# Optimization experiments

Measured on AMD Instinct MI355X. Metric: run time of the kernel, lower is better.

The kernel has to match this reference:

```python
import jax, jax.numpy as jnp
import numpy as np

L, H, C, V, B, T = 8, 12, 576, 16389, 2, 1024
HD = C // H


def _ln(h, w, b):
    mu = h.mean(-1, keepdims=True)
    var = ((h - mu) ** 2).mean(-1, keepdims=True)
    return (h - mu) * jax.lax.rsqrt(var + 1e-5) * w + b


def _forward(idx, wte, W_qkv, W_o, ln1_w, ln1_b, ln2_w, ln2_b, lambdas, W_gate, W_up, W_down, lnf_w, lnf_b):
    Bi, Ti = idx.shape
    scale = 1.0 / np.sqrt(HD).astype(np.float32)
    x = wte[idx]                          # [B,T,C] token embedding
    x0 = x                                # embed shortcut
    # value residual v1: third chunk of layer-0 c_attn applied to raw embeddings (no LN)
    qkv0 = x @ W_qkv[0].T                 # [B,T,3C]
    v1 = qkv0[..., 2 * C:].reshape(Bi, Ti, H, HD).transpose(0, 2, 1, 3)  # [B,H,T,hd]
    # ALiBi slopes: 1/x^(i+1), x = 256^(1/H)  ->  2^(-8(i+1)/H)
    slopes = 2.0 ** (-8.0 * jnp.arange(1, H + 1, dtype=jnp.float32) / H)
    r = jnp.arange(Ti)
    # (i - j).clamp(min=0) with i=cols, j=rows (zero on causal region, as in source)
    alibi = jnp.maximum(r[None, :] - r[:, None], 0).astype(jnp.float32)[None] * slopes[:, None, None]  # [H,T,T]
    causal = (r[None, :] <= r[:, None])[None, None]  # [1,1,T,T]

    def block(x, p):
        Wq, Wo, l1w, l1b, l2w, l2b, lam, Wg, Wu, Wd = p
        x = lam[0] * x + lam[1] * x0
        h = _ln(x, l1w, l1b)
        qkv = h @ Wq.T
        q, k, v = jnp.split(qkv, 3, axis=-1)
        q = q.reshape(Bi, Ti, H, HD).transpose(0, 2, 1, 3)
        k = k.reshape(Bi, Ti, H, HD).transpose(0, 2, 1, 3)
        v = v.reshape(Bi, Ti, H, HD).transpose(0, 2, 1, 3)
        v = 0.5 * v + 0.5 * v1               # value residual (fixed lambda)
        att = jnp.einsum('bhqd,bhkd->bhqk', q, k) * scale + alibi[None]
        att = jnp.where(causal, att, -jnp.inf)
        att = jax.nn.softmax(att, axis=-1)
        y = jnp.einsum('bhqk,bhkd->bhqd', att, v).transpose(0, 2, 1, 3).reshape(Bi, Ti, C)
        x = x + y @ Wo.T
        h2 = _ln(x, l2w, l2b)
        x = x + (jax.nn.gelu(h2 @ Wg.T, approximate=True) * (h2 @ Wu.T)) @ Wd.T  # GEGLU
        return x, None

    x, _ = jax.lax.scan(block, x, (W_qkv, W_o, ln1_w, ln1_b, ln2_w, ln2_b, lambdas, W_gate, W_up, W_down))
    x = _ln(x, lnf_w, lnf_b)
    logits = x @ wte.T                    # tied lm_head
    return 30.0 * jnp.tanh(logits / 30.0)  # logit_clamp


def setup_inputs() -> dict:
    key = jax.random.key(0)
    ks = jax.random.split(key, 8)
    s = 0.02
    return {
        'idx': jax.random.randint(ks[0], (B, T), 0, V, dtype=jnp.int32),
        'wte': s * jax.random.normal(ks[1], (V, C), jnp.float32),
        'W_qkv': s * jax.random.normal(ks[2], (L, 3 * C, C), jnp.float32),
        'W_o': s * jax.random.normal(ks[3], (L, C, C), jnp.float32),
        'ln1_w': jnp.ones((L, C), jnp.float32),
        'ln1_b': jnp.zeros((L, C), jnp.float32),
        'ln2_w': jnp.ones((L, C), jnp.float32),
        'ln2_b': jnp.zeros((L, C), jnp.float32),
        'lambdas': jnp.tile(jnp.array([1.0, 0.0], jnp.float32), (L, 1)),
        'W_gate': s * jax.random.normal(ks[4], (L, 2 * C, C), jnp.float32),
        'W_up': s * jax.random.normal(ks[5], (L, 2 * C, C), jnp.float32),
        'W_down': s * jax.random.normal(ks[6], (L, C, 2 * C), jnp.float32),
        'lnf_w': jnp.ones((C,), jnp.float32),
        'lnf_b': jnp.zeros((C,), jnp.float32),
    }


def reference(idx, wte, W_qkv, W_o, ln1_w, ln1_b, ln2_w, ln2_b, lambdas, W_gate, W_up, W_down, lnf_w, lnf_b):
    return _forward(idx, wte, W_qkv, W_o, ln1_w, ln1_b, ln2_w, ln2_b, lambdas, W_gate, W_up, W_down, lnf_w, lnf_b)
```

## Files before the change

kernel.cpp:

```cpp
#include <hip/hip_runtime.h>
#include <hip/hip_bf16.h>
#include <stdint.h>
#include <stddef.h>

#define NL 8
#define NH 12
#define CC 576
#define VV 16389
#define TT 1024
#define HD 48
#define BT 2048
#define C3 1728
#define C2 1152

typedef __attribute__((ext_vector_type(4))) float f32x4;
typedef __attribute__((ext_vector_type(8))) __bf16 bf16x8;
typedef __attribute__((ext_vector_type(8))) unsigned short u16x8;

static __device__ __forceinline__ unsigned short f2bf(float f) {
  __hip_bfloat16 h = __float2bfloat16(f);
  return __builtin_bit_cast(unsigned short, h);
}
static __device__ __forceinline__ float bf2f(unsigned short u) {
  __hip_bfloat16 h = __builtin_bit_cast(__hip_bfloat16, u);
  return __bfloat162float(h);
}
static __device__ __forceinline__ float gelu_tanh(float g) {
  float t = tanhf(0.7978845608028654f * (g + 0.044715f * g * g * g));
  return 0.5f * g * (1.f + t);
}

__global__ void cvt_kernel(const float* __restrict__ in, unsigned short* __restrict__ out, int n4) {
  int i = blockIdx.x * blockDim.x + threadIdx.x;
  int stride = gridDim.x * blockDim.x;
  for (; i < n4; i += stride) {
    float4 v = reinterpret_cast<const float4*>(in)[i];
    ushort4 o;
    o.x = f2bf(v.x); o.y = f2bf(v.y); o.z = f2bf(v.z); o.w = f2bf(v.w);
    reinterpret_cast<ushort4*>(out)[i] = o;
  }
}

__global__ void cvt_gu_kernel(const float* __restrict__ g, const float* __restrict__ u,
                              unsigned short* __restrict__ out, int n4) {
  int i = blockIdx.x * blockDim.x + threadIdx.x;
  int stride = gridDim.x * blockDim.x;
  const int per_l = C2 * (CC / 4);
  for (; i < n4; i += stride) {
    int l = i / per_l, rem = i - l * per_l;
    int j = rem / (CC / 4), c4 = rem - j * (CC / 4);
    float4 gv = reinterpret_cast<const float4*>(g)[i];
    float4 uv = reinterpret_cast<const float4*>(u)[i];
    ushort4 go, uo;
    go.x = f2bf(gv.x); go.y = f2bf(gv.y); go.z = f2bf(gv.z); go.w = f2bf(gv.w);
    uo.x = f2bf(uv.x); uo.y = f2bf(uv.y); uo.z = f2bf(uv.z); uo.w = f2bf(uv.w);
    size_t dst = ((size_t)l * 2 * C2 + 2 * j) * CC + c4 * 4;
    *reinterpret_cast<ushort4*>(out + dst) = go;
    *reinterpret_cast<ushort4*>(out + dst + CC) = uo;
  }
}

__global__ void embed_kernel(const int* __restrict__ idx, const float* __restrict__ wte,
                             float* __restrict__ x, float* __restrict__ x0,
                             unsigned short* __restrict__ xbf) {
  int t = blockIdx.x;
  int tok = idx[t];
  const float* src = wte + (size_t)tok * CC;
  size_t base = (size_t)t * CC;
  for (int c = threadIdx.x; c < CC; c += blockDim.x) {
    float v = src[c];
    x[base + c] = v;
    x0[base + c] = v;
    xbf[base + c] = f2bf(v);
  }
}

template<int MIX>
__global__ __launch_bounds__(256) void ln_kernel(
    const float* __restrict__ xin, const float* __restrict__ x0,
    const float* __restrict__ lam, const float* __restrict__ w,
    const float* __restrict__ b, float* __restrict__ xmix,
    unsigned short* __restrict__ hbf) {
  int row = blockIdx.x * 4 + (threadIdx.x >> 6);
  int lane = threadIdx.x & 63;
  size_t base = (size_t)row * CC;
  float lam0 = 1.f, lam1 = 0.f;
  if (MIX) { lam0 = lam[0]; lam1 = lam[1]; }
  float e[9];
  float s = 0.f;
#pragma unroll
  for (int j = 0; j < 9; ++j) {
    int c = lane + 64 * j;
    float v = xin[base + c];
    if (MIX) v = lam0 * v + lam1 * x0[base + c];
    e[j] = v; s += v;
  }
#pragma unroll
  for (int mm = 1; mm < 64; mm <<= 1) s += __shfl_xor(s, mm, 64);
  float mu = s * (1.f / 576.f);
  float var = 0.f;
#pragma unroll
  for (int j = 0; j < 9; ++j) { float d = e[j] - mu; var += d * d; }
#pragma unroll
  for (int mm = 1; mm < 64; mm <<= 1) var += __shfl_xor(var, mm, 64);
  float rstd = 1.f / sqrtf(var * (1.f / 576.f) + 1e-5f);
#pragma unroll
  for (int j = 0; j < 9; ++j) {
    int c = lane + 64 * j;
    if (MIX) xmix[base + c] = e[j];
    hbf[base + c] = f2bf((e[j] - mu) * rstd * w[c] + b[c]);
  }
}

template<int EPI, int BN>
__global__ __launch_bounds__(256) void gemm_bt(
    const unsigned short* __restrict__ X, const unsigned short* __restrict__ W,
    float* __restrict__ Cf, unsigned short* __restrict__ Cb,
    unsigned short* __restrict__ Cb2, const unsigned short* __restrict__ v1b,
    int N, int K) {
  constexpr int PB = BN / 32;
  constexpr int NI = BN / 32;
  __shared__ unsigned short As[128 * 64];
  __shared__ unsigned short Bs[BN * 64];
  const int tid = threadIdx.x;
  const int lane = tid & 63;
  const int wv = tid >> 6;
  const int wr = wv >> 1, wc = wv & 1;
  const int nwg = gridDim.x;
  const int bid = blockIdx.x;
  const int swz = (bid & 7) * (nwg >> 3) + (bid >> 3);
  const int m0 = (swz & 15) * 128;
  const int n0 = (swz >> 4) * BN;
  const int l15 = lane & 15, g = lane >> 4;
  const int trow = tid >> 3;
  const int tcb = (tid & 7) << 4;

  const unsigned short* xrow[4];
  const unsigned short* wrow[PB];
  int aoff[4], boff[PB];
#pragma unroll
  for (int p = 0; p < 4; ++p) {
    int r = p * 32 + trow;
    xrow[p] = X + (size_t)(m0 + r) * K + (tcb >> 1);
    aoff[p] = r * 128 + (tcb ^ ((trow & 7) << 4));
  }
#pragma unroll
  for (int p = 0; p < PB; ++p) {
    int r = p * 32 + trow;
    int rn = n0 + r; if (rn > N - 1) rn = N - 1;
    wrow[p] = W + (size_t)rn * K + (tcb >> 1);
    boff[p] = r * 128 + (tcb ^ ((trow & 7) << 4));
  }
  const int rdswz = (l15 & 7) << 4;

  f32x4 acc[4][NI];
  const f32x4 fz = {0.f, 0.f, 0.f, 0.f};
#pragma unroll
  for (int i = 0; i < 4; ++i)
#pragma unroll
    for (int j = 0; j < NI; ++j) acc[i][j] = fz;

  u16x8 stg[4 + PB];
#pragma unroll
  for (int p = 0; p < 4; ++p) stg[p] = *reinterpret_cast<const u16x8*>(xrow[p]);
#pragma unroll
  for (int p = 0; p < PB; ++p) stg[4 + p] = *reinterpret_cast<const u16x8*>(wrow[p]);

  for (int k0 = 0; k0 < K; k0 += 64) {
    __syncthreads();
#pragma unroll
    for (int p = 0; p < 4; ++p)
      *reinterpret_cast<u16x8*>(reinterpret_cast<char*>(As) + aoff[p]) = stg[p];
#pragma unroll
    for (int p = 0; p < PB; ++p)
      *reinterpret_cast<u16x8*>(reinterpret_cast<char*>(Bs) + boff[p]) = stg[4 + p];
    __syncthreads();
    if (k0 + 64 < K) {
#pragma unroll
      for (int p = 0; p < 4; ++p)
        stg[p] = *reinterpret_cast<const u16x8*>(xrow[p] + k0 + 64);
#pragma unroll
      for (int p = 0; p < PB; ++p)
        stg[4 + p] = *reinterpret_cast<const u16x8*>(wrow[p] + k0 + 64);
    }
#pragma unroll
    for (int kk = 0; kk < 2; ++kk) {
      const int kbyte = kk * 64 + g * 16;
      bf16x8 a[4], bb[NI];
#pragma unroll
      for (int mi = 0; mi < 4; ++mi) {
        int ar = wr * 64 + mi * 16 + l15;
        a[mi] = *reinterpret_cast<const bf16x8*>(
            reinterpret_cast<const char*>(As) + ar * 128 + (kbyte ^ rdswz));
      }
#pragma unroll
      for (int ni = 0; ni < NI; ++ni) {
        int br = wc * (BN / 2) + ni * 16 + l15;
        bb[ni] = *reinterpret_cast<const bf16x8*>(
            reinterpret_cast<const char*>(Bs) + br * 128 + (kbyte ^ rdswz));
      }
#pragma unroll
      for (int mi = 0; mi < 4; ++mi)
#pragma unroll
        for (int ni = 0; ni < NI; ++ni)
          acc[mi][ni] = __builtin_amdgcn_mfma_f32_16x16x32_bf16(a[mi], bb[ni], acc[mi][ni], 0, 0, 0);
    }
  }
#pragma unroll
  for (int mi = 0; mi < 4; ++mi) {
#pragma unroll
    for (int ni = 0; ni < NI; ++ni) {
      int gn = n0 + wc * (BN / 2) + ni * 16 + l15;
      int gm = m0 + wr * 64 + mi * 16 + g * 4;
#pragma unroll
      for (int r = 0; r < 4; ++r) {
        float v = acc[mi][ni][r];
        size_t row = (size_t)(gm + r);
        if (EPI == 5) {
          float partner = __shfl_xor(v, 1, 64);
          if ((l15 & 1) == 0 && gn < N)
            Cb[row * (N / 2) + (gn >> 1)] = f2bf(gelu_tanh(v) * partner);
        } else if (gn < N) {
          if (EPI == 0) Cf[row * N + gn] = v;
          else if (EPI == 1) Cf[row * N + gn] += v;
          else if (EPI == 2) Cf[row * N + gn] = 30.f * tanhf(v * (1.f / 30.f));
          else if (EPI == 3) Cb[row * N + gn] = f2bf(v);
          else if (EPI == 4) {
            if (gn < C2) Cb[row * C2 + gn] = f2bf(v);
            else Cb2[row * CC + (gn - C2)] = f2bf(0.5f * v + 0.5f * bf2f(v1b[row * CC + (gn - C2)]));
          }
        }
      }
    }
  }
}

__global__ __launch_bounds__(256) void attn_kernel(
    const unsigned short* __restrict__ qkb, const unsigned short* __restrict__ vmix,
    unsigned short* __restrict__ ybf) {
  __shared__ unsigned short Kl[64 * 56];
  __shared__ unsigned short Vt[48 * 72];
  __shared__ unsigned short Pl[4][16 * 72];
  const int bid = blockIdx.x;
  const int swz = (bid & 7) * 48 + (bid >> 3);
  const int qb = swz & 15, bh = swz >> 4;
  const int b = bh / NH, h = bh % NH;
  const int tid = threadIdx.x, lane = tid & 63, wv = tid >> 6;
  const int l15 = lane & 15, g = lane >> 4;
  const int rb = b * TT;
  const int q0 = qb * 64 + wv * 16;
  const float scale = 0.14433756729740643f;

  bf16x8 qa[2];
  {
    const unsigned short* qp = qkb + (size_t)(rb + q0 + l15) * C2 + h * HD;
    qa[0] = *reinterpret_cast<const bf16x8*>(qp + 8 * g);
    if (g < 2) qa[1] = *reinterpret_cast<const bf16x8*>(qp + 32 + 8 * g);
    else { u16x8 z = {0,0,0,0,0,0,0,0}; qa[1] = __builtin_bit_cast(bf16x8, z); }
  }

  float mrow[4], lrow[4];
  f32x4 o[3];
  const f32x4 fz = {0.f, 0.f, 0.f, 0.f};
#pragma unroll
  for (int r = 0; r < 4; ++r) { mrow[r] = -1e30f; lrow[r] = 0.f; }
  o[0] = fz; o[1] = fz; o[2] = fz;

  for (int kb = 0; kb <= qb; ++kb) {
    __syncthreads();
#pragma unroll
    for (int jj = 0; jj < 3; ++jj) {
      int fi = tid + 256 * jj;
      int r = fi / 12, dq = (fi % 12) * 4;
      *reinterpret_cast<ushort4*>(&Kl[r * 56 + dq]) =
          *reinterpret_cast<const ushort4*>(qkb + (size_t)(rb + kb * 64 + r) * C2 + CC + h * HD + dq);
    }
#pragma unroll
    for (int jj = 0; jj < 12; ++jj) {
      int e = tid + 256 * jj;
      int r = e / 48, d = e - r * 48;
      Vt[d * 72 + r] = vmix[(size_t)(rb + kb * 64 + r) * CC + h * HD + d];
    }
    __syncthreads();

    f32x4 s[4];
    s[0] = fz; s[1] = fz; s[2] = fz; s[3] = fz;
#pragma unroll
    for (int c = 0; c < 2; ++c) {
#pragma unroll
      for (int t4 = 0; t4 < 4; ++t4) {
        bf16x8 kf;
        if (c == 1 && g >= 2) {
          u16x8 z = {0,0,0,0,0,0,0,0};
          kf = __builtin_bit_cast(bf16x8, z);
        } else {
          kf = *reinterpret_cast<const bf16x8*>(&Kl[(t4 * 16 + l15) * 56 + c * 32 + 8 * g]);
        }
        s[t4] = __builtin_amdgcn_mfma_f32_16x16x32_bf16(qa[c], kf, s[t4], 0, 0, 0);
      }
    }
#pragma unroll
    for (int t4 = 0; t4 < 4; ++t4) s[t4] *= scale;
    if (kb == qb) {
#pragma unroll
      for (int t4 = 0; t4 < 4; ++t4) {
        int key = kb * 64 + t4 * 16 + l15;
#pragma unroll
        for (int r = 0; r < 4; ++r)
          if (key > q0 + g * 4 + r) s[t4][r] = -1e30f;
      }
    }
    float pv[4][4];
#pragma unroll
    for (int r = 0; r < 4; ++r) {
      float tm = fmaxf(fmaxf(s[0][r], s[1][r]), fmaxf(s[2][r], s[3][r]));
#pragma unroll
      for (int mm = 1; mm < 16; mm <<= 1) tm = fmaxf(tm, __shfl_xor(tm, mm, 64));
      float mnew = fmaxf(mrow[r], tm);
      float cf = __expf(mrow[r] - mnew);
      lrow[r] *= cf;
      o[0][r] *= cf; o[1][r] *= cf; o[2][r] *= cf;
      mrow[r] = mnew;
      float rs = 0.f;
#pragma unroll
      for (int t4 = 0; t4 < 4; ++t4) {
        float pe = __expf(s[t4][r] - mnew);
        pv[t4][r] = pe; rs += pe;
      }
#pragma unroll
      for (int mm = 1; mm < 16; mm <<= 1) rs += __shfl_xor(rs, mm, 64);
      lrow[r] += rs;
    }
#pragma unroll
    for (int t4 = 0; t4 < 4; ++t4)
#pragma unroll
      for (int r = 0; r < 4; ++r)
        Pl[wv][(g * 4 + r) * 72 + t4 * 16 + l15] = f2bf(pv[t4][r]);
#pragma unroll
    for (int c = 0; c < 2; ++c) {
      bf16x8 pa = *reinterpret_cast<const bf16x8*>(&Pl[wv][l15 * 72 + c * 32 + 8 * g]);
#pragma unroll
      for (int dt = 0; dt < 3; ++dt) {
        bf16x8 vb = *reinterpret_cast<const bf16x8*>(&Vt[(dt * 16 + l15) * 72 + c * 32 + 8 * g]);
        o[dt] = __builtin_amdgcn_mfma_f32_16x16x32_bf16(pa, vb, o[dt], 0, 0, 0);
      }
    }
  }
#pragma unroll
  for (int r = 0; r < 4; ++r) {
    float inv = 1.f / lrow[r];
    int tr = q0 + g * 4 + r;
#pragma unroll
    for (int dt = 0; dt < 3; ++dt)
      ybf[(size_t)(rb + tr) * CC + h * HD + dt * 16 + l15] = f2bf(o[dt][r] * inv);
  }
}

extern "C" void kernel_launch(void* const* d_in, const int* in_sizes, int n_in,
                              void* d_out, int out_size, void* d_ws, size_t ws_size,
                              hipStream_t stream) {
  (void)in_sizes; (void)n_in; (void)out_size; (void)ws_size;
  const int*   idx  = (const int*)d_in[0];
  const float* wte  = (const float*)d_in[1];
  const float* Wqkv = (const float*)d_in[2];
  const float* Wo   = (const float*)d_in[3];
  const float* ln1w = (const float*)d_in[4];
  const float* ln1b = (const float*)d_in[5];
  const float* ln2w = (const float*)d_in[6];
  const float* ln2b = (const float*)d_in[7];
  const float* lam  = (const float*)d_in[8];
  const float* Wg   = (const float*)d_in[9];
  const float* Wu   = (const float*)d_in[10];
  const float* Wd   = (const float*)d_in[11];
  const float* lnfw = (const float*)d_in[12];
  const float* lnfb = (const float*)d_in[13];
  float* out = (float*)d_out;

  char* ws = (char*)d_ws;
  size_t off = 0;
  auto alloc = [&](size_t bytes) -> void* {
    void* p = ws + off;
    off = (off + bytes + 255) & ~(size_t)255;
    return p;
  };
  unsigned short* wqkv_b = (unsigned short*)alloc((size_t)NL * C3 * CC * 2);
  unsigned short* wo_b   = (unsigned short*)alloc((size_t)NL * CC * CC * 2);
  unsigned short* wgu_b  = (unsigned short*)alloc((size_t)NL * 2 * C2 * CC * 2);
  unsigned short* wd_b   = (unsigned short*)alloc((size_t)NL * CC * C2 * 2);
  unsigned short* wte_b  = (unsigned short*)alloc((size_t)VV * CC * 2);
  float* x     = (float*)alloc((size_t)BT * CC * 4);
  float* x0    = (float*)alloc((size_t)BT * CC * 4);
  unsigned short* hb    = (unsigned short*)alloc((size_t)BT * CC * 2);
  unsigned short* qkb   = (unsigned short*)alloc((size_t)BT * C2 * 2);
  unsigned short* v1b   = (unsigned short*)alloc((size_t)BT * CC * 2);
  unsigned short* vmixb = (unsigned short*)alloc((size_t)BT * CC * 2);
  unsigned short* yb    = (unsigned short*)alloc((size_t)BT * CC * 2);
  unsigned short* gub   = (unsigned short*)alloc((size_t)BT * C2 * 2);

  auto cvt = [&](const float* in, unsigned short* o, size_t n) {
    cvt_kernel<<<dim3(2048), 256, 0, stream>>>(in, o, (int)(n / 4));
  };
  cvt(Wqkv, wqkv_b, (size_t)NL * C3 * CC);
  cvt(Wo,   wo_b,   (size_t)NL * CC * CC);
  cvt(Wd,   wd_b,   (size_t)NL * CC * C2);
  cvt(wte,  wte_b,  (size_t)VV * CC);
  cvt_gu_kernel<<<dim3(2048), 256, 0, stream>>>(Wg, Wu, wgu_b, NL * C2 * (CC / 4));

  embed_kernel<<<dim3(BT), 256, 0, stream>>>(idx, wte, x, x0, hb);

  auto nb = [](int N, int BN) { return (N + BN - 1) / BN; };
  gemm_bt<3, 64><<<dim3(16 * nb(CC, 64)), 256, 0, stream>>>(
      hb, wqkv_b + (size_t)C2 * CC, nullptr, v1b, nullptr, nullptr, CC, CC);

  for (int l = 0; l < NL; ++l) {
    ln_kernel<1><<<dim3(512), 256, 0, stream>>>(x, x0, lam + 2 * l, ln1w + l * CC, ln1b + l * CC, x, hb);
    gemm_bt<4, 128><<<dim3(16 * nb(C3, 128)), 256, 0, stream>>>(
        hb, wqkv_b + (size_t)l * C3 * CC, nullptr, qkb, vmixb, v1b, C3, CC);
    attn_kernel<<<dim3(16 * 24), 256, 0, stream>>>(qkb, vmixb, yb);
    gemm_bt<1, 64><<<dim3(16 * nb(CC, 64)), 256, 0, stream>>>(
        yb, wo_b + (size_t)l * CC * CC, x, nullptr, nullptr, nullptr, CC, CC);
    ln_kernel<0><<<dim3(512), 256, 0, stream>>>(x, nullptr, nullptr, ln2w + l * CC, ln2b + l * CC, nullptr, hb);
    gemm_bt<5, 128><<<dim3(16 * nb(2 * C2, 128)), 256, 0, stream>>>(
        hb, wgu_b + (size_t)l * 2 * C2 * CC, nullptr, gub, nullptr, nullptr, 2 * C2, CC);
    gemm_bt<1, 64><<<dim3(16 * nb(CC, 64)), 256, 0, stream>>>(
        gub, wd_b + (size_t)l * CC * C2, x, nullptr, nullptr, nullptr, CC, C2);
  }

  ln_kernel<0><<<dim3(512), 256, 0, stream>>>(x, nullptr, nullptr, lnfw, lnfb, nullptr, hb);
  gemm_bt<2, 128><<<dim3(16 * nb(VV, 128)), 256, 0, stream>>>(
      hb, wte_b, out, nullptr, nullptr, nullptr, VV, CC);
}
```

Measured before the change: 1.359 ms.

## Fuse LayerNorm into GEMM A-operand loads and use 64x64 tiles for narrow GEMMs

Removes the separate LayerNorm kernels. Each GEMM block now computes per-row mean and rstd for its M tile from the fp32 residual and applies normalisation while loading the A tile, converting to bf16 on the fly. The residual mix output goes to a ping-pong buffer to avoid read/write races across blocks. Narrow N=576 GEMMs switch to 64x64 tiles to double the grid size. The cost is redundant LN statistics and fp32 A loads in every N-tile block (up to 129 blocks for the lm_head), plus the extra reads of x0.

New measurement: 2.009 ms. +47.8%, slower.

```diff
diff --git a/kernel.cpp b/kernel.cpp
--- a/kernel.cpp
+++ b/kernel.cpp
@@ -75,53 +75,27 @@
   }
 }
 
-template<int MIX>
-__global__ __launch_bounds__(256) void ln_kernel(
-    const float* __restrict__ xin, const float* __restrict__ x0,
-    const float* __restrict__ lam, const float* __restrict__ w,
-    const float* __restrict__ b, float* __restrict__ xmix,
-    unsigned short* __restrict__ hbf) {
-  int row = blockIdx.x * 4 + (threadIdx.x >> 6);
-  int lane = threadIdx.x & 63;
-  size_t base = (size_t)row * CC;
-  float lam0 = 1.f, lam1 = 0.f;
-  if (MIX) { lam0 = lam[0]; lam1 = lam[1]; }
-  float e[9];
-  float s = 0.f;
-#pragma unroll
-  for (int j = 0; j < 9; ++j) {
-    int c = lane + 64 * j;
-    float v = xin[base + c];
-    if (MIX) v = lam0 * v + lam1 * x0[base + c];
-    e[j] = v; s += v;
-  }
-#pragma unroll
-  for (int mm = 1; mm < 64; mm <<= 1) s += __shfl_xor(s, mm, 64);
-  float mu = s * (1.f / 576.f);
-  float var = 0.f;
-#pragma unroll
-  for (int j = 0; j < 9; ++j) { float d = e[j] - mu; var += d * d; }
-#pragma unroll
-  for (int mm = 1; mm < 64; mm <<= 1) var += __shfl_xor(var, mm, 64);
-  float rstd = 1.f / sqrtf(var * (1.f / 576.f) + 1e-5f);
-#pragma unroll
-  for (int j = 0; j < 9; ++j) {
-    int c = lane + 64 * j;
-    if (MIX) xmix[base + c] = e[j];
-    hbf[base + c] = f2bf((e[j] - mu) * rstd * w[c] + b[c]);
-  }
-}
-
-template<int EPI, int BN>
+template<int EPI, int BM, int BN, int LNA>
 __global__ __launch_bounds__(256) void gemm_bt(
-    const unsigned short* __restrict__ X, const unsigned short* __restrict__ W,
+    const unsigned short* __restrict__ Xb, const float* __restrict__ Xf,
+    const float* __restrict__ X0, const float* __restrict__ lam,
+    const float* __restrict__ lnw, const float* __restrict__ lnb,
+    float* __restrict__ xmixout,
+    const unsigned short* __restrict__ W,
     float* __restrict__ Cf, unsigned short* __restrict__ Cb,
     unsigned short* __restrict__ Cb2, const unsigned short* __restrict__ v1b,
     int N, int K) {
+  constexpr int NMB = BT / BM;
+  constexpr int PA = BM / 32;
   constexpr int PB = BN / 32;
+  constexpr int MI = BM / 32;
   constexpr int NI = BN / 32;
-  __shared__ unsigned short As[128 * 64];
+  __shared__ unsigned short As[BM * 64];
   __shared__ unsigned short Bs[BN * 64];
+  __shared__ float MuS[(LNA > 0) ? BM : 1];
+  __shared__ float RsS[(LNA > 0) ? BM : 1];
+  __shared__ float WbS[(LNA > 0) ? CC : 1];
+  __shared__ float BbS[(LNA > 0) ? CC : 1];
   const int tid = threadIdx.x;
   const int lane = tid & 63;
   const int wv = tid >> 6;
@@ -129,19 +103,78 @@
   const int nwg = gridDim.x;
   const int bid = blockIdx.x;
   const int swz = (bid & 7) * (nwg >> 3) + (bid >> 3);
-  const int m0 = (swz & 15) * 128;
-  const int n0 = (swz >> 4) * BN;
+  const int m0 = (swz % NMB) * BM;
+  const int n0 = (swz / NMB) * BN;
   const int l15 = lane & 15, g = lane >> 4;
   const int trow = tid >> 3;
   const int tcb = (tid & 7) << 4;
 
-  const unsigned short* xrow[4];
+  float lam0 = 1.f, lam1 = 0.f;
+  if (LNA == 1) { lam0 = lam[0]; lam1 = lam[1]; }
+
+  if (LNA > 0) {
+    for (int c = tid; c < CC; c += 256) { WbS[c] = lnw[c]; BbS[c] = lnb[c]; }
+    for (int rr = 0; rr < BM / 4; ++rr) {
+      int r = wv * (BM / 4) + rr;
+      size_t grow = (size_t)(m0 + r) * CC;
+      float e[9];
+      float s = 0.f;
+#pragma unroll
+      for (int j = 0; j < 9; ++j) {
+        int c = lane + 64 * j;
+        float v = Xf[grow + c];
+        if (LNA == 1) v = lam0 * v + lam1 * X0[grow + c];
+        e[j] = v; s += v;
+      }
+#pragma unroll
+      for (int mm = 1; mm < 64; mm <<= 1) s += __shfl_xor(s, mm, 64);
+      float mu = s * (1.f / 576.f);
+      float var = 0.f;
+#pragma unroll
+      for (int j = 0; j < 9; ++j) { float d = e[j] - mu; var += d * d; }
+#pragma unroll
+      for (int mm = 1; mm < 64; mm <<= 1) var += __shfl_xor(var, mm, 64);
+      float rstd = 1.f / sqrtf(var * (1.f / 576.f) + 1e-5f);
+      if (lane == 0) { MuS[r] = mu; RsS[r] = rstd; }
+      if (LNA == 1 && n0 == 0) {
+#pragma unroll
+        for (int j = 0; j < 9; ++j) xmixout[grow + lane + 64 * j] = e[j];
+      }
+    }
+    __syncthreads();
+  }
+
+  auto ldA = [&](int p, int k) -> u16x8 {
+    int r = p * 32 + trow;
+    int c0 = (tid & 7) * 8;
+    if (LNA == 0) {
+      return *reinterpret_cast<const u16x8*>(Xb + (size_t)(m0 + r) * K + c0 + k);
+    } else {
+      size_t base = (size_t)(m0 + r) * CC + c0 + k;
+      float4 a0 = *reinterpret_cast<const float4*>(Xf + base);
+      float4 a1 = *reinterpret_cast<const float4*>(Xf + base + 4);
+      float ev[8] = {a0.x, a0.y, a0.z, a0.w, a1.x, a1.y, a1.z, a1.w};
+      if (LNA == 1) {
+        float4 b0 = *reinterpret_cast<const float4*>(X0 + base);
+        float4 b1 = *reinterpret_cast<const float4*>(X0 + base + 4);
+        float bv[8] = {b0.x, b0.y, b0.z, b0.w, b1.x, b1.y, b1.z, b1.w};
+#pragma unroll
+        for (int i = 0; i < 8; ++i) ev[i] = lam0 * ev[i] + lam1 * bv[i];
+      }
+      float mu = MuS[r], rs = RsS[r];
+      union { u16x8 v; unsigned short u[8]; } o;
+#pragma unroll
+      for (int i = 0; i < 8; ++i)
+        o.u[i] = f2bf((ev[i] - mu) * rs * WbS[c0 + k + i] + BbS[c0 + k + i]);
+      return o.v;
+    }
+  };
+
   const unsigned short* wrow[PB];
-  int aoff[4], boff[PB];
-#pragma unroll
-  for (int p = 0; p < 4; ++p) {
+  int aoff[PA], boff[PB];
+#pragma unroll
+  for (int p = 0; p < PA; ++p) {
     int r = p * 32 + trow;
-    xrow[p] = X + (size_t)(m0 + r) * K + (tcb >> 1);
     aoff[p] = r * 128 + (tcb ^ ((trow & 7) << 4));
   }
 #pragma unroll
@@ -153,43 +186,42 @@
   }
   const int rdswz = (l15 & 7) << 4;
 
-  f32x4 acc[4][NI];
+  f32x4 acc[MI][NI];
   const f32x4 fz = {0.f, 0.f, 0.f, 0.f};
 #pragma unroll
-  for (int i = 0; i < 4; ++i)
+  for (int i = 0; i < MI; ++i)
 #pragma unroll
     for (int j = 0; j < NI; ++j) acc[i][j] = fz;
 
-  u16x8 stg[4 + PB];
-#pragma unroll
-  for (int p = 0; p < 4; ++p) stg[p] = *reinterpret_cast<const u16x8*>(xrow[p]);
-#pragma unroll
-  for (int p = 0; p < PB; ++p) stg[4 + p] = *reinterpret_cast<const u16x8*>(wrow[p]);
+  u16x8 stg[PA + PB];
+#pragma unroll
+  for (int p = 0; p < PA; ++p) stg[p] = ldA(p, 0);
+#pragma unroll
+  for (int p = 0; p < PB; ++p) stg[PA + p] = *reinterpret_cast<const u16x8*>(wrow[p]);
 
   for (int k0 = 0; k0 < K; k0 += 64) {
     __syncthreads();
 #pragma unroll
-    for (int p = 0; p < 4; ++p)
+    for (int p = 0; p < PA; ++p)
       *reinterpret_cast<u16x8*>(reinterpret_cast<char*>(As) + aoff[p]) = stg[p];
 #pragma unroll
     for (int p = 0; p < PB; ++p)
-      *reinterpret_cast<u16x8*>(reinterpret_cast<char*>(Bs) + boff[p]) = stg[4 + p];
+      *reinterpret_cast<u16x8*>(reinterpret_cast<char*>(Bs) + boff[p]) = stg[PA + p];
     __syncthreads();
     if (k0 + 64 < K) {
 #pragma unroll
-      for (int p = 0; p < 4; ++p)
-        stg[p] = *reinterpret_cast<const u16x8*>(xrow[p] + k0 + 64);
+      for (int p = 0; p < PA; ++p) stg[p] = ldA(p, k0 + 64);
 #pragma unroll
       for (int p = 0; p < PB; ++p)
-        stg[4 + p] = *reinterpret_cast<const u16x8*>(wrow[p] + k0 + 64);
+        stg[PA + p] = *reinterpret_cast<const u16x8*>(wrow[p] + k0 + 64);
     }
 #pragma unroll
     for (int kk = 0; kk < 2; ++kk) {
       const int kbyte = kk * 64 + g * 16;
-      bf16x8 a[4], bb[NI];
-#pragma unroll
-      for (int mi = 0; mi < 4; ++mi) {
-        int ar = wr * 64 + mi * 16 + l15;
+      bf16x8 a[MI], bb[NI];
+#pragma unroll
+      for (int mi = 0; mi < MI; ++mi) {
+        int ar = wr * (BM / 2) + mi * 16 + l15;
         a[mi] = *reinterpret_cast<const bf16x8*>(
             reinterpret_cast<const char*>(As) + ar * 128 + (kbyte ^ rdswz));
       }
@@ -200,18 +232,18 @@
             reinterpret_cast<const char*>(Bs) + br * 128 + (kbyte ^ rdswz));
       }
 #pragma unroll
-      for (int mi = 0; mi < 4; ++mi)
+      for (int mi = 0; mi < MI; ++mi)
 #pragma unroll
         for (int ni = 0; ni < NI; ++ni)
           acc[mi][ni] = __builtin_amdgcn_mfma_f32_16x16x32_bf16(a[mi], bb[ni], acc[mi][ni], 0, 0, 0);
     }
   }
 #pragma unroll
-  for (int mi = 0; mi < 4; ++mi) {
+  for (int mi = 0; mi < MI; ++mi) {
 #pragma unroll
     for (int ni = 0; ni < NI; ++ni) {
       int gn = n0 + wc * (BN / 2) + ni * 16 + l15;
-      int gm = m0 + wr * 64 + mi * 16 + g * 4;
+      int gm = m0 + wr * (BM / 2) + mi * 16 + g * 4;
 #pragma unroll
       for (int r = 0; r < 4; ++r) {
         float v = acc[mi][ni][r];
@@ -388,8 +420,10 @@
   unsigned short* wgu_b  = (unsigned short*)alloc((size_t)NL * 2 * C2 * CC * 2);
   unsigned short* wd_b   = (unsigned short*)alloc((size_t)NL * CC * C2 * 2);
   unsigned short* wte_b  = (unsigned short*)alloc((size_t)VV * CC * 2);
-  float* x     = (float*)alloc((size_t)BT * CC * 4);
-  float* x0    = (float*)alloc((size_t)BT * CC * 4);
+  float* xe  = (float*)alloc((size_t)BT * CC * 4);
+  float* x0  = (float*)alloc((size_t)BT * CC * 4);
+  float* xb1 = (float*)alloc((size_t)BT * CC * 4);
+  float* xb2 = (float*)alloc((size_t)BT * CC * 4);
   unsigned short* hb    = (unsigned short*)alloc((size_t)BT * CC * 2);
   unsigned short* qkb   = (unsigned short*)alloc((size_t)BT * C2 * 2);
   unsigned short* v1b   = (unsigned short*)alloc((size_t)BT * CC * 2);
@@ -406,27 +440,34 @@
   cvt(wte,  wte_b,  (size_t)VV * CC);
   cvt_gu_kernel<<<dim3(2048), 256, 0, stream>>>(Wg, Wu, wgu_b, NL * C2 * (CC / 4));
 
-  embed_kernel<<<dim3(BT), 256, 0, stream>>>(idx, wte, x, x0, hb);
+  embed_kernel<<<dim3(BT), 256, 0, stream>>>(idx, wte, xe, x0, hb);
 
   auto nb = [](int N, int BN) { return (N + BN - 1) / BN; };
-  gemm_bt<3, 64><<<dim3(16 * nb(CC, 64)), 256, 0, stream>>>(
-      hb, wqkv_b + (size_t)C2 * CC, nullptr, v1b, nullptr, nullptr, CC, CC);
-
+  gemm_bt<3, 64, 64, 0><<<dim3(32 * nb(CC, 64)), 256, 0, stream>>>(
+      hb, nullptr, nullptr, nullptr, nullptr, nullptr, nullptr,
+      wqkv_b + (size_t)C2 * CC, nullptr, v1b, nullptr, nullptr, CC, CC);
+
+  float* cur = xe;
+  float* nxt = xb1;
   for (int l = 0; l < NL; ++l) {
-    ln_kernel<1><<<dim3(512), 256, 0, stream>>>(x, x0, lam + 2 * l, ln1w + l * CC, ln1b + l * CC, x, hb);
-    gemm_bt<4, 128><<<dim3(16 * nb(C3, 128)), 256, 0, stream>>>(
-        hb, wqkv_b + (size_t)l * C3 * CC, nullptr, qkb, vmixb, v1b, C3, CC);
+    gemm_bt<4, 128, 128, 1><<<dim3(16 * nb(C3, 128)), 256, 0, stream>>>(
+        nullptr, cur, x0, lam + 2 * l, ln1w + l * CC, ln1b + l * CC, nxt,
+        wqkv_b + (size_t)l * C3 * CC, nullptr, qkb, vmixb, v1b, C3, CC);
     attn_kernel<<<dim3(16 * 24), 256, 0, stream>>>(qkb, vmixb, yb);
-    gemm_bt<1, 64><<<dim3(16 * nb(CC, 64)), 256, 0, stream>>>(
-        yb, wo_b + (size_t)l * CC * CC, x, nullptr, nullptr, nullptr, CC, CC);
-    ln_kernel<0><<<dim3(512), 256, 0, stream>>>(x, nullptr, nullptr, ln2w + l * CC, ln2b + l * CC, nullptr, hb);
-    gemm_bt<5, 128><<<dim3(16 * nb(2 * C2, 128)), 256, 0, stream>>>(
-        hb, wgu_b + (size_t)l * 2 * C2 * CC, nullptr, gub, nullptr, nullptr, 2 * C2, CC);
-    gemm_bt<1, 64><<<dim3(16 * nb(CC, 64)), 256, 0, stream>>>(
-        gub, wd_b + (size_t)l * CC * C2, x, nullptr, nullptr, nullptr, CC, C2);
-  }
-
-  ln_kernel<0><<<dim3(512), 256, 0, stream>>>(x, nullptr, nullptr, lnfw, lnfb, nullptr, hb);
-  gemm_bt<2, 128><<<dim3(16 * nb(VV, 128)), 256, 0, stream>>>(
-      hb, wte_b, out, nullptr, nullptr, nullptr, VV, CC);
-}
+    gemm_bt<1, 64, 64, 0><<<dim3(32 * nb(CC, 64)), 256, 0, stream>>>(
+        yb, nullptr, nullptr, nullptr, nullptr, nullptr, nullptr,
+        wo_b + (size_t)l * CC * CC, nxt, nullptr, nullptr, nullptr, CC, CC);
+    gemm_bt<5, 128, 128, 2><<<dim3(16 * nb(2 * C2, 128)), 256, 0, stream>>>(
+        nullptr, nxt, nullptr, nullptr, ln2w + l * CC, ln2b + l * CC, nullptr,
+        wgu_b + (size_t)l * 2 * C2 * CC, nullptr, gub, nullptr, nullptr, 2 * C2, CC);
+    gemm_bt<1, 64, 64, 0><<<dim3(32 * nb(CC, 64)), 256, 0, stream>>>(
+        gub, nullptr, nullptr, nullptr, nullptr, nullptr, nullptr,
+        wd_b + (size_t)l * CC * C2, nxt, nullptr, nullptr, nullptr, CC, C2);
+    cur = nxt;
+    nxt = (cur == xb1) ? xb2 : xb1;
+  }
+
+  gemm_bt<2, 128, 128, 2><<<dim3(16 * nb(VV, 128)), 256, 0, stream>>>(
+      nullptr, cur, nullptr, nullptr, lnfw, lnfb, nullptr,
+      wte_b, out, nullptr, nullptr, nullptr, VV, CC);
+}
```

## Double-buffer attention K/V tiles, schedule heavy query blocks first, shrink GEMM M-tiles

Applied to the files above, without the earlier changes.

The attention kernel now double-buffers its K and V shared-memory tiles, prefetching the next key block while the current one is computed. It also vectorizes the V transpose loads and launches the longest causal query blocks first for better load balance. The GEMM gains a BM template parameter, and the per-layer GEMMs switch to 64-row tiles, doubling the number of workgroups to fill more compute units. The costs are more shared memory per attention block and less data reuse per GEMM tile.

After: 1.145 ms. 15.7% less time.

```diff
diff --git a/kernel.cpp b/kernel.cpp
--- a/kernel.cpp
+++ b/kernel.cpp
@@ -112,15 +112,18 @@
   }
 }
 
-template<int EPI, int BN>
+template<int EPI, int BM, int BN>
 __global__ __launch_bounds__(256) void gemm_bt(
     const unsigned short* __restrict__ X, const unsigned short* __restrict__ W,
     float* __restrict__ Cf, unsigned short* __restrict__ Cb,
     unsigned short* __restrict__ Cb2, const unsigned short* __restrict__ v1b,
     int N, int K) {
+  constexpr int NMB = BT / BM;
+  constexpr int PA = BM / 32;
   constexpr int PB = BN / 32;
+  constexpr int MI = BM / 32;
   constexpr int NI = BN / 32;
-  __shared__ unsigned short As[128 * 64];
+  __shared__ unsigned short As[BM * 64];
   __shared__ unsigned short Bs[BN * 64];
   const int tid = threadIdx.x;
   const int lane = tid & 63;
@@ -129,17 +132,17 @@
   const int nwg = gridDim.x;
   const int bid = blockIdx.x;
   const int swz = (bid & 7) * (nwg >> 3) + (bid >> 3);
-  const int m0 = (swz & 15) * 128;
-  const int n0 = (swz >> 4) * BN;
+  const int m0 = (swz % NMB) * BM;
+  const int n0 = (swz / NMB) * BN;
   const int l15 = lane & 15, g = lane >> 4;
   const int trow = tid >> 3;
   const int tcb = (tid & 7) << 4;
 
-  const unsigned short* xrow[4];
+  const unsigned short* xrow[PA];
   const unsigned short* wrow[PB];
-  int aoff[4], boff[PB];
-#pragma unroll
-  for (int p = 0; p < 4; ++p) {
+  int aoff[PA], boff[PB];
+#pragma unroll
+  for (int p = 0; p < PA; ++p) {
     int r = p * 32 + trow;
     xrow[p] = X + (size_t)(m0 + r) * K + (tcb >> 1);
     aoff[p] = r * 128 + (tcb ^ ((trow & 7) << 4));
@@ -153,43 +156,43 @@
   }
   const int rdswz = (l15 & 7) << 4;
 
-  f32x4 acc[4][NI];
+  f32x4 acc[MI][NI];
   const f32x4 fz = {0.f, 0.f, 0.f, 0.f};
 #pragma unroll
-  for (int i = 0; i < 4; ++i)
+  for (int i = 0; i < MI; ++i)
 #pragma unroll
     for (int j = 0; j < NI; ++j) acc[i][j] = fz;
 
-  u16x8 stg[4 + PB];
-#pragma unroll
-  for (int p = 0; p < 4; ++p) stg[p] = *reinterpret_cast<const u16x8*>(xrow[p]);
-#pragma unroll
-  for (int p = 0; p < PB; ++p) stg[4 + p] = *reinterpret_cast<const u16x8*>(wrow[p]);
+  u16x8 stg[PA + PB];
+#pragma unroll
+  for (int p = 0; p < PA; ++p) stg[p] = *reinterpret_cast<const u16x8*>(xrow[p]);
+#pragma unroll
+  for (int p = 0; p < PB; ++p) stg[PA + p] = *reinterpret_cast<const u16x8*>(wrow[p]);
 
   for (int k0 = 0; k0 < K; k0 += 64) {
     __syncthreads();
 #pragma unroll
-    for (int p = 0; p < 4; ++p)
+    for (int p = 0; p < PA; ++p)
       *reinterpret_cast<u16x8*>(reinterpret_cast<char*>(As) + aoff[p]) = stg[p];
 #pragma unroll
     for (int p = 0; p < PB; ++p)
-      *reinterpret_cast<u16x8*>(reinterpret_cast<char*>(Bs) + boff[p]) = stg[4 + p];
+      *reinterpret_cast<u16x8*>(reinterpret_cast<char*>(Bs) + boff[p]) = stg[PA + p];
     __syncthreads();
     if (k0 + 64 < K) {
 #pragma unroll
-      for (int p = 0; p < 4; ++p)
+      for (int p = 0; p < PA; ++p)
         stg[p] = *reinterpret_cast<const u16x8*>(xrow[p] + k0 + 64);
 #pragma unroll
       for (int p = 0; p < PB; ++p)
-        stg[4 + p] = *reinterpret_cast<const u16x8*>(wrow[p] + k0 + 64);
+        stg[PA + p] = *reinterpret_cast<const u16x8*>(wrow[p] + k0 + 64);
     }
 #pragma unroll
     for (int kk = 0; kk < 2; ++kk) {
       const int kbyte = kk * 64 + g * 16;
-      bf16x8 a[4], bb[NI];
-#pragma unroll
-      for (int mi = 0; mi < 4; ++mi) {
-        int ar = wr * 64 + mi * 16 + l15;
+      bf16x8 a[MI], bb[NI];
+#pragma unroll
+      for (int mi = 0; mi < MI; ++mi) {
+        int ar = wr * (BM / 2) + mi * 16 + l15;
         a[mi] = *reinterpret_cast<const bf16x8*>(
             reinterpret_cast<const char*>(As) + ar * 128 + (kbyte ^ rdswz));
       }
@@ -200,18 +203,18 @@
             reinterpret_cast<const char*>(Bs) + br * 128 + (kbyte ^ rdswz));
       }
 #pragma unroll
-      for (int mi = 0; mi < 4; ++mi)
+      for (int mi = 0; mi < MI; ++mi)
 #pragma unroll
         for (int ni = 0; ni < NI; ++ni)
           acc[mi][ni] = __builtin_amdgcn_mfma_f32_16x16x32_bf16(a[mi], bb[ni], acc[mi][ni], 0, 0, 0);
     }
   }
 #pragma unroll
-  for (int mi = 0; mi < 4; ++mi) {
+  for (int mi = 0; mi < MI; ++mi) {
 #pragma unroll
     for (int ni = 0; ni < NI; ++ni) {
       int gn = n0 + wc * (BN / 2) + ni * 16 + l15;
-      int gm = m0 + wr * 64 + mi * 16 + g * 4;
+      int gm = m0 + wr * (BM / 2) + mi * 16 + g * 4;
 #pragma unroll
       for (int r = 0; r < 4; ++r) {
         float v = acc[mi][ni][r];
@@ -238,12 +241,12 @@
 __global__ __launch_bounds__(256) void attn_kernel(
     const unsigned short* __restrict__ qkb, const unsigned short* __restrict__ vmix,
     unsigned short* __restrict__ ybf) {
-  __shared__ unsigned short Kl[64 * 56];
-  __shared__ unsigned short Vt[48 * 72];
+  __shared__ unsigned short Kl[2][64 * 56];
+  __shared__ unsigned short Vt[2][48 * 72];
   __shared__ unsigned short Pl[4][16 * 72];
   const int bid = blockIdx.x;
-  const int swz = (bid & 7) * 48 + (bid >> 3);
-  const int qb = swz & 15, bh = swz >> 4;
+  const int qb = 15 - (bid / 24);
+  const int bh = bid % 24;
   const int b = bh / NH, h = bh % NH;
   const int tid = threadIdx.x, lane = tid & 63, wv = tid >> 6;
   const int l15 = lane & 15, g = lane >> 4;
@@ -251,6 +254,27 @@
   const int q0 = qb * 64 + wv * 16;
   const float scale = 0.14433756729740643f;
 
+  auto stage = [&](int kb, int buf) {
+    const int r0 = rb + kb * 64;
+#pragma unroll
+    for (int jj = 0; jj < 3; ++jj) {
+      int fi = tid + 256 * jj;
+      int r = fi / 12, dq = (fi % 12) * 4;
+      *reinterpret_cast<ushort4*>(&Kl[buf][r * 56 + dq]) =
+          *reinterpret_cast<const ushort4*>(qkb + (size_t)(r0 + r) * C2 + CC + h * HD + dq);
+    }
+#pragma unroll
+    for (int jj = 0; jj < 3; ++jj) {
+      int e4 = tid + 256 * jj;
+      int r = e4 / 12, d4 = (e4 % 12) * 4;
+      ushort4 v = *reinterpret_cast<const ushort4*>(vmix + (size_t)(r0 + r) * CC + h * HD + d4);
+      Vt[buf][(d4 + 0) * 72 + r] = v.x;
+      Vt[buf][(d4 + 1) * 72 + r] = v.y;
+      Vt[buf][(d4 + 2) * 72 + r] = v.z;
+      Vt[buf][(d4 + 3) * 72 + r] = v.w;
+    }
+  };
+
   bf16x8 qa[2];
   {
     const unsigned short* qp = qkb + (size_t)(rb + q0 + l15) * C2 + h * HD;
@@ -266,22 +290,12 @@
   for (int r = 0; r < 4; ++r) { mrow[r] = -1e30f; lrow[r] = 0.f; }
   o[0] = fz; o[1] = fz; o[2] = fz;
 
+  stage(0, 0);
+  __syncthreads();
+
   for (int kb = 0; kb <= qb; ++kb) {
-    __syncthreads();
-#pragma unroll
-    for (int jj = 0; jj < 3; ++jj) {
-      int fi = tid + 256 * jj;
-      int r = fi / 12, dq = (fi % 12) * 4;
-      *reinterpret_cast<ushort4*>(&Kl[r * 56 + dq]) =
-          *reinterpret_cast<const ushort4*>(qkb + (size_t)(rb + kb * 64 + r) * C2 + CC + h * HD + dq);
-    }
-#pragma unroll
-    for (int jj = 0; jj < 12; ++jj) {
-      int e = tid + 256 * jj;
-      int r = e / 48, d = e - r * 48;
-      Vt[d * 72 + r] = vmix[(size_t)(rb + kb * 64 + r) * CC + h * HD + d];
-    }
-    __syncthreads();
+    const int cur = kb & 1;
+    if (kb < qb) stage(kb + 1, cur ^ 1);
 
     f32x4 s[4];
     s[0] = fz; s[1] = fz; s[2] = fz; s[3] = fz;
@@ -294,7 +308,7 @@
           u16x8 z = {0,0,0,0,0,0,0,0};
           kf = __builtin_bit_cast(bf16x8, z);
         } else {
-          kf = *reinterpret_cast<const bf16x8*>(&Kl[(t4 * 16 + l15) * 56 + c * 32 + 8 * g]);
+          kf = *reinterpret_cast<const bf16x8*>(&Kl[cur][(t4 * 16 + l15) * 56 + c * 32 + 8 * g]);
         }
         s[t4] = __builtin_amdgcn_mfma_f32_16x16x32_bf16(qa[c], kf, s[t4], 0, 0, 0);
       }
@@ -341,10 +355,11 @@
       bf16x8 pa = *reinterpret_cast<const bf16x8*>(&Pl[wv][l15 * 72 + c * 32 + 8 * g]);
 #pragma unroll
       for (int dt = 0; dt < 3; ++dt) {
-        bf16x8 vb = *reinterpret_cast<const bf16x8*>(&Vt[(dt * 16 + l15) * 72 + c * 32 + 8 * g]);
+        bf16x8 vb = *reinterpret_cast<const bf16x8*>(&Vt[cur][(dt * 16 + l15) * 72 + c * 32 + 8 * g]);
         o[dt] = __builtin_amdgcn_mfma_f32_16x16x32_bf16(pa, vb, o[dt], 0, 0, 0);
       }
     }
+    __syncthreads();
   }
 #pragma unroll
   for (int r = 0; r < 4; ++r) {
@@ -388,8 +403,8 @@
   unsigned short* wgu_b  = (unsigned short*)alloc((size_t)NL * 2 * C2 * CC * 2);
   unsigned short* wd_b   = (unsigned short*)alloc((size_t)NL * CC * C2 * 2);
   unsigned short* wte_b  = (unsigned short*)alloc((size_t)VV * CC * 2);
-  float* x     = (float*)alloc((size_t)BT * CC * 4);
-  float* x0    = (float*)alloc((size_t)BT * CC * 4);
+  float* x   = (float*)alloc((size_t)BT * CC * 4);
+  float* x0  = (float*)alloc((size_t)BT * CC * 4);
   unsigned short* hb    = (unsigned short*)alloc((size_t)BT * CC * 2);
   unsigned short* qkb   = (unsigned short*)alloc((size_t)BT * C2 * 2);
   unsigned short* v1b   = (unsigned short*)alloc((size_t)BT * CC * 2);
@@ -409,24 +424,24 @@
   embed_kernel<<<dim3(BT), 256, 0, stream>>>(idx, wte, x, x0, hb);
 
   auto nb = [](int N, int BN) { return (N + BN - 1) / BN; };
-  gemm_bt<3, 64><<<dim3(16 * nb(CC, 64)), 256, 0, stream>>>(
+  gemm_bt<3, 64, 64><<<dim3(32 * nb(CC, 64)), 256, 0, stream>>>(
       hb, wqkv_b + (size_t)C2 * CC, nullptr, v1b, nullptr, nullptr, CC, CC);
 
   for (int l = 0; l < NL; ++l) {
     ln_kernel<1><<<dim3(512), 256, 0, stream>>>(x, x0, lam + 2 * l, ln1w + l * CC, ln1b + l * CC, x, hb);
-    gemm_bt<4, 128><<<dim3(16 * nb(C3, 128)), 256, 0, stream>>>(
+    gemm_bt<4, 64, 128><<<dim3(32 * nb(C3, 128)), 256, 0, stream>>>(
         hb, wqkv_b + (size_t)l * C3 * CC, nullptr, qkb, vmixb, v1b, C3, CC);
     attn_kernel<<<dim3(16 * 24), 256, 0, stream>>>(qkb, vmixb, yb);
-    gemm_bt<1, 64><<<dim3(16 * nb(CC, 64)), 256, 0, stream>>>(
+    gemm_bt<1, 64, 64><<<dim3(32 * nb(CC, 64)), 256, 0, stream>>>(
         yb, wo_b + (size_t)l * CC * CC, x, nullptr, nullptr, nullptr, CC, CC);
     ln_kernel<0><<<dim3(512), 256, 0, stream>>>(x, nullptr, nullptr, ln2w + l * CC, ln2b + l * CC, nullptr, hb);
-    gemm_bt<5, 128><<<dim3(16 * nb(2 * C2, 128)), 256, 0, stream>>>(
+    gemm_bt<5, 64, 128><<<dim3(32 * nb(2 * C2, 128)), 256, 0, stream>>>(
         hb, wgu_b + (size_t)l * 2 * C2 * CC, nullptr, gub, nullptr, nullptr, 2 * C2, CC);
-    gemm_bt<1, 64><<<dim3(16 * nb(CC, 64)), 256, 0, stream>>>(
+    gemm_bt<1, 64, 64><<<dim3(32 * nb(CC, 64)), 256, 0, stream>>>(
         gub, wd_b + (size_t)l * CC * C2, x, nullptr, nullptr, nullptr, CC, C2);
   }
 
   ln_kernel<0><<<dim3(512), 256, 0, stream>>>(x, nullptr, nullptr, lnfw, lnfb, nullptr, hb);
-  gemm_bt<2, 128><<<dim3(16 * nb(VV, 128)), 256, 0, stream>>>(
+  gemm_bt<2, 128, 128><<<dim3(16 * nb(VV, 128)), 256, 0, stream>>>(
       hb, wte_b, out, nullptr, nullptr, nullptr, VV, CC);
 }
```
